# Kernel tuning notes

Measured on AMD Instinct MI355X. Metric: run time of the kernel, lower is better.

## Reference

```python
import jax, jax.numpy as jnp
import numpy as np

D_MODEL = 3072
N_HEADS = 24
MAX_LEN = 2048
ROPE_THETA = 10000.0
DH = D_MODEL // N_HEADS                  # 128
Q_PROJ = D_MODEL // 2                    # 1536
KV_PROJ = 2 * D_MODEL // 3               # 2048
NOPE = DH // 2                           # 64
ROPE = DH // 2                           # 64
EPS = 1e-5


def layernorm(x, w, b):
    m = jnp.mean(x, axis=-1, keepdims=True)
    v = jnp.mean(jnp.square(x - m), axis=-1, keepdims=True)
    return (x - m) / jnp.sqrt(v + EPS) * w + b


def rotate_half(x):
    h = x.shape[-1] // 2
    return jnp.concatenate([-x[..., h:], x[..., :h]], axis=-1)


def rope_tables(S):
    freqs = 1.0 / ROPE_THETA ** (jnp.arange(0, DH, 2, dtype=jnp.float32) / DH)  # [DH/2]
    emb = jnp.arange(S, dtype=jnp.float32)[:, None] * freqs[None, :]            # [S, DH/2]
    # torch: take first ROPE//2 freqs then .repeat(...,2) => tile along last axis
    cos = jnp.tile(jnp.cos(emb)[:, : ROPE // 2], (1, 2))  # [S, ROPE]
    sin = jnp.tile(jnp.sin(emb)[:, : ROPE // 2], (1, 2))
    return cos[None, None], sin[None, None]               # [1,1,S,ROPE]


def setup_inputs() -> dict:
    key = jax.random.key(0)
    ks = jax.random.split(key, 7)
    x = jax.random.normal(ks[0], (2, 2048, D_MODEL), dtype=jnp.float32)
    p = lambda k, shp: 0.01 * jax.random.normal(k, shp, dtype=jnp.float32)
    return {
        "x": x,
        "W_dq": p(ks[1], (D_MODEL, Q_PROJ)),
        "W_uq": p(ks[2], (Q_PROJ, D_MODEL)),
        "q_ln_w": jnp.ones((Q_PROJ,), jnp.float32),
        "q_ln_b": jnp.zeros((Q_PROJ,), jnp.float32),
        "W_dkv": p(ks[3], (D_MODEL, KV_PROJ + ROPE)),
        "W_ukv": p(ks[4], (KV_PROJ, D_MODEL + N_HEADS * NOPE)),
        "kv_ln_w": jnp.ones((KV_PROJ,), jnp.float32),
        "kv_ln_b": jnp.zeros((KV_PROJ,), jnp.float32),
        "W_o": p(ks[5], (D_MODEL, D_MODEL)),
    }


def reference(x, W_dq, W_uq, q_ln_w, q_ln_b, W_dkv, W_ukv, kv_ln_w, kv_ln_b, W_o):
    B, S, D = x.shape
    cos, sin = rope_tables(S)  # past_length=0, S_full=S

    # Q path: low-rank down/up projection
    cq = layernorm(x @ W_dq, q_ln_w, q_ln_b)          # [B,S,Q_PROJ]
    Q = (cq @ W_uq).reshape(B, S, N_HEADS, DH).transpose(0, 2, 1, 3)  # [B,H,S,DH]
    Q_nope, Q_rope = Q[..., :NOPE], Q[..., NOPE:]
    Q_rope = Q_rope * cos + rotate_half(Q_rope) * sin

    # KV path
    compressed_kv = x @ W_dkv                          # [B,S,KV_PROJ+ROPE]
    KV_lora = layernorm(compressed_kv[..., :KV_PROJ], kv_ln_w, kv_ln_b)
    K_rope = compressed_kv[..., KV_PROJ:]              # [B,S,ROPE]
    KV = (KV_lora @ W_ukv).reshape(B, S, N_HEADS, DH + NOPE).transpose(0, 2, 1, 3)
    K_nope, V = KV[..., :NOPE], KV[..., NOPE:]         # [B,H,S,NOPE], [B,H,S,DH]

    K_rope = K_rope[:, None]                           # [B,1,S,ROPE] shared head
    K_rope = K_rope * cos + rotate_half(K_rope) * sin

    q = jnp.concatenate([Q_nope, Q_rope], axis=-1)     # [B,H,S,DH]
    # k = cat(K_nope, K_rope broadcast over heads)
    k = jnp.concatenate([K_nope, jnp.broadcast_to(K_rope, (B, N_HEADS, S, ROPE))], axis=-1)

    scale = 1.0 / jnp.sqrt(jnp.float32(DH))
    scores = jnp.einsum("bhqd,bhkd->bhqk", q, k) * scale
    causal = jnp.tril(jnp.ones((S, S), dtype=bool))
    scores = jnp.where(causal[None, None], scores, jnp.float32(-jnp.inf))
    attn = jax.nn.softmax(scores, axis=-1)
    out = jnp.einsum("bhqk,bhkd->bhqd", attn, V)
    out = out.transpose(0, 2, 1, 3).reshape(B, S, D)
    out = out @ W_o.T
    return out, compressed_kv
```

## Files before the change

kernel.cpp:

```cpp
#include <hip/hip_runtime.h>

typedef unsigned short u16;
typedef __attribute__((ext_vector_type(8))) short short8;
typedef __attribute__((ext_vector_type(4))) float f32x4;

#define NROWS   4096
#define S_LEN   2048
#define NHEADS  24
#define DMODEL  3072
#define QPROJ   1536
#define KVPROJ  2048
#define CKV_W   2112
#define UKV_N   4608

__device__ __forceinline__ float bf2f(u16 v) {
    unsigned u = ((unsigned)v) << 16; float f; __builtin_memcpy(&f, &u, 4); return f;
}
__device__ __forceinline__ u16 f2bf(float f) {
    unsigned u; __builtin_memcpy(&u, &f, 4);
    u = (u + 0x7FFFu + ((u >> 16) & 1u)) >> 16; return (u16)u;
}
__device__ __forceinline__ void async16(const u16* g, u16* l) {
    __builtin_amdgcn_global_load_lds((const __attribute__((address_space(1))) unsigned int*)g,
                                     (__attribute__((address_space(3))) unsigned int*)l,
                                     16, 0, 0);
}

__global__ void conv_bf16(const float* __restrict__ X, u16* __restrict__ Y, int n) {
    int i = (blockIdx.x * 256 + threadIdx.x) * 4;
    if (i >= n) return;
    float4 v = *(const float4*)(X + i);
    Y[i+0] = f2bf(v.x); Y[i+1] = f2bf(v.y); Y[i+2] = f2bf(v.z); Y[i+3] = f2bf(v.w);
}

__global__ void transpose_bf16(const float* __restrict__ W, u16* __restrict__ WT,
                               int K, int N, float scale) {
    __shared__ float t[32][33];
    int nb = blockIdx.x * 32, kb = blockIdx.y * 32;
    int c = threadIdx.x & 31, rq = threadIdx.x >> 5;
#pragma unroll
    for (int i = 0; i < 4; ++i) {
        int r = rq * 4 + i;
        t[r][c] = W[(size_t)(kb + r) * N + nb + c];
    }
    __syncthreads();
#pragma unroll
    for (int i = 0; i < 4; ++i) {
        int r = rq * 4 + i;
        WT[(size_t)(nb + r) * K + kb + c] = f2bf(t[c][r] * scale);
    }
}

__global__ __launch_bounds__(256) void ln_kernel(const float* __restrict__ X, int ldx,
                                                 const float* __restrict__ g,
                                                 const float* __restrict__ b,
                                                 u16* __restrict__ Y, int W) {
    int row = blockIdx.x;
    const float4* x4 = (const float4*)(X + (size_t)row * ldx);
    int W4 = W >> 2;
    float s = 0.f, s2 = 0.f;
    for (int i = threadIdx.x; i < W4; i += 256) {
        float4 v = x4[i];
        s += v.x + v.y + v.z + v.w;
        s2 += v.x * v.x + v.y * v.y + v.z * v.z + v.w * v.w;
    }
#pragma unroll
    for (int off = 32; off >= 1; off >>= 1) { s += __shfl_xor(s, off); s2 += __shfl_xor(s2, off); }
    __shared__ float red[8];
    int w = threadIdx.x >> 6;
    if ((threadIdx.x & 63) == 0) { red[w] = s; red[4 + w] = s2; }
    __syncthreads();
    s  = red[0] + red[1] + red[2] + red[3];
    s2 = red[4] + red[5] + red[6] + red[7];
    float mean = s / W;
    float var  = s2 / W - mean * mean;
    float rstd = rsqrtf(var + 1e-5f);
    const float4* g4 = (const float4*)g;
    const float4* b4 = (const float4*)b;
    u16* y = Y + (size_t)row * W;
    for (int i = threadIdx.x; i < W4; i += 256) {
        float4 v = x4[i], gg = g4[i], bb = b4[i];
        u16 o[4];
        o[0] = f2bf((v.x - mean) * rstd * gg.x + bb.x);
        o[1] = f2bf((v.y - mean) * rstd * gg.y + bb.y);
        o[2] = f2bf((v.z - mean) * rstd * gg.z + bb.z);
        o[3] = f2bf((v.w - mean) * rstd * gg.w + bb.w);
        *(ulong1*)&y[i * 4] = *(ulong1*)o;
    }
}

__global__ void rope_q_kernel(u16* __restrict__ Q) {
    int idx = blockIdx.x * 256 + threadIdx.x;
    int j = idx & 31; int t = idx >> 5; int h = t % NHEADS; int row = t / NHEADS;
    int s = row & (S_LEN - 1);
    float freq = __expf(-(float)j * (9.210340371976184f / 64.f));
    float ang = (float)s * freq;
    float c = cosf(ang), si = sinf(ang);
    u16* p = Q + (size_t)row * DMODEL + h * 128 + 64;
    float x1 = bf2f(p[j]), x2 = bf2f(p[j + 32]);
    p[j]      = f2bf(x1 * c - x2 * si);
    p[j + 32] = f2bf(x2 * c + x1 * si);
}

__global__ void rope_k_kernel(const float* __restrict__ ckv, u16* __restrict__ kr) {
    int idx = blockIdx.x * 256 + threadIdx.x;
    int j = idx & 31; int row = idx >> 5;
    int s = row & (S_LEN - 1);
    float freq = __expf(-(float)j * (9.210340371976184f / 64.f));
    float ang = (float)s * freq;
    float c = cosf(ang), si = sinf(ang);
    const float* src = ckv + (size_t)row * CKV_W + KVPROJ;
    float x1 = src[j], x2 = src[j + 32];
    kr[(size_t)row * 64 + j]      = f2bf(x1 * c - x2 * si);
    kr[(size_t)row * 64 + j + 32] = f2bf(x2 * c + x1 * si);
}

__global__ __launch_bounds__(256) void pack_k(const u16* __restrict__ KVb,
                                              const u16* __restrict__ kr,
                                              u16* __restrict__ Kp) {
    int bh = blockIdx.y, bb = bh / NHEADS, h = bh % NHEADS;
    int s0 = blockIdx.x * 64;
    int t = threadIdx.x;
    size_t base = (size_t)bb * S_LEN;
#pragma unroll
    for (int it = 0; it < 4; ++it) {
        int j = it * 256 + t;
        int r = j >> 4, cb = (j & 15) * 8;
        int s = s0 + r;
        uint4 v;
        if (cb < 64) v = *(const uint4*)&KVb[(base + s) * UKV_N + h * 192 + cb];
        else         v = *(const uint4*)&kr[(base + s) * 64 + (cb - 64)];
        *(uint4*)&Kp[((size_t)bh * S_LEN + s) * 128 + cb] = v;
    }
}

__global__ __launch_bounds__(256) void pack_v(const u16* __restrict__ KVb,
                                              u16* __restrict__ Vt) {
    __shared__ u16 tile[64][136];
    int bh = blockIdx.y, bb = bh / NHEADS, h = bh % NHEADS;
    int s0 = blockIdx.x * 64;
    int t = threadIdx.x;
    size_t base = (size_t)bb * S_LEN;
#pragma unroll
    for (int it = 0; it < 4; ++it) {
        int j = it * 256 + t;
        int r = j >> 4, cb = (j & 15) * 8;
        *(uint4*)&tile[r][cb] = *(const uint4*)&KVb[(base + s0 + r) * UKV_N + h * 192 + 64 + cb];
    }
    __syncthreads();
#pragma unroll
    for (int it = 0; it < 4; ++it) {
        int j = it * 256 + t;
        int d = j >> 3, sb = (j & 7) * 8;
        u16 tmp[8];
#pragma unroll
        for (int e = 0; e < 8; ++e) tmp[e] = tile[sb + e][d];
        *(uint4*)&Vt[((size_t)bh * 128 + d) * S_LEN + s0 + sb] = *(uint4*)tmp;
    }
}

template<bool OUT_BF16>
__global__ __launch_bounds__(256) void gemm_nt(const u16* __restrict__ A,
                                               const u16* __restrict__ B,
                                               void* __restrict__ Cv,
                                               int M, int N, int K, int nx) {
    __shared__ u16 a_lds[2][128][32];
    __shared__ u16 b_lds[2][128][32];
    int nwg = (int)gridDim.x;
    int bid = (int)blockIdx.x;
    int wg = (bid & 7) * (nwg >> 3) + (bid >> 3);
    int by = wg / nx, bx = wg - by * nx;
    int m0 = by * 128, n0 = bx * 128;
    int tid = threadIdx.x, lane = tid & 63, w = tid >> 6;
    int wm = w >> 1, wn = w & 1;
    int srow = lane >> 2;
    int kx = (lane >> 4) & 2;
    int scol = ((lane & 3) ^ kx) * 8;
    int r0 = w * 32 + srow, r1 = w * 32 + 16 + srow;
    const u16* A0 = A + (size_t)(m0 + r0) * K + scol;
    const u16* A1 = A + (size_t)(m0 + r1) * K + scol;
    int bn0 = n0 + r0; if (bn0 >= N) bn0 = N - 1;
    int bn1 = n0 + r1; if (bn1 >= N) bn1 = N - 1;
    const u16* B0 = B + (size_t)bn0 * K + scol;
    const u16* B1 = B + (size_t)bn1 * K + scol;
    char* aB = (char*)&a_lds[0][0][0];
    char* bB = (char*)&b_lds[0][0][0];
    int d0 = w * 2048, d1 = w * 2048 + 1024;
    int cb = ((lane >> 4) * 16) ^ ((lane & 8) << 2);

    f32x4 acc[4][4] = {};
    async16(A0, (u16*)(aB + d0)); async16(A1, (u16*)(aB + d1));
    async16(B0, (u16*)(bB + d0)); async16(B1, (u16*)(bB + d1));
    __syncthreads();
    int buf = 0;
    for (int kb = 0; kb < K; kb += 32) {
        if (kb + 32 < K) {
            int ob = (buf ^ 1) * 8192;
            async16(A0 + kb + 32, (u16*)(aB + ob + d0));
            async16(A1 + kb + 32, (u16*)(aB + ob + d1));
            async16(B0 + kb + 32, (u16*)(bB + ob + d0));
            async16(B1 + kb + 32, (u16*)(bB + ob + d1));
        }
        const char* ab = aB + buf * 8192;
        const char* bb = bB + buf * 8192;
        short8 af[4], bf[4];
#pragma unroll
        for (int i = 0; i < 4; ++i) {
            af[i] = *(const short8*)(ab + (wm * 64 + i * 16 + (lane & 15)) * 64 + cb);
            bf[i] = *(const short8*)(bb + (wn * 64 + i * 16 + (lane & 15)) * 64 + cb);
        }
#pragma unroll
        for (int i = 0; i < 4; ++i)
#pragma unroll
            for (int j = 0; j < 4; ++j)
                acc[i][j] = __builtin_amdgcn_mfma_f32_16x16x32_bf16(af[i], bf[j], acc[i][j], 0, 0, 0);
        __syncthreads();
        buf ^= 1;
    }
#pragma unroll
    for (int i = 0; i < 4; ++i) {
        int row = m0 + wm * 64 + i * 16 + ((lane >> 4) << 2);
#pragma unroll
        for (int j = 0; j < 4; ++j) {
            int col = n0 + wn * 64 + j * 16 + (lane & 15);
            if (col < N) {
#pragma unroll
                for (int r = 0; r < 4; ++r) {
                    if (OUT_BF16) ((u16*)Cv)[(size_t)(row + r) * N + col] = f2bf(acc[i][j][r]);
                    else          ((float*)Cv)[(size_t)(row + r) * N + col] = acc[i][j][r];
                }
            }
        }
    }
}

__global__ __launch_bounds__(256) void attn_kernel(const u16* __restrict__ Qb,
                                                   const u16* __restrict__ Kp,
                                                   const u16* __restrict__ Vt,
                                                   u16* __restrict__ AO) {
    __shared__ u16 k_lds[64][128];
    __shared__ u16 v_lds[128][64];
    __shared__ u16 p_lds[4][16][64];
    int bid = blockIdx.x;
    int jj = bid >> 3;
    int bh = (bid & 7) * 6 + (jj >> 4);
    int bx = jj & 15;
    int bb = bh / NHEADS, h = bh % NHEADS;
    int tid = threadIdx.x, lane = tid & 63, w = tid >> 6;
    size_t base = (size_t)bb * S_LEN;
    size_t bhS = (size_t)bh * S_LEN;

    const char* Kbyte = (const char*)Kp;
    const char* Vbyte = (const char*)Vt;
    char* kB = (char*)&k_lds[0][0];
    char* vB = (char*)&v_lds[0][0];
    char* pB = (char*)&p_lds[0][0][0] + w * 2048;
    size_t ksrc[4], vsrc[4];
    int kd[4];
#pragma unroll
    for (int is = 0; is < 4; ++is) {
        int j = is * 256 + tid;
        int r = j >> 4;
        int cbs = ((j & 15) * 16) ^ ((r & 7) << 4);
        ksrc[is] = (bhS + r) * 256 + cbs;
        int d = j >> 3;
        int kbs = (((j & 7) ^ (d & 7)) * 16);
        vsrc[is] = ((size_t)bh * 128 + d) * (S_LEN * 2) + kbs;
        kd[is] = (is * 256 + w * 64) * 16;
    }

    for (int seg = 0; seg < 2; ++seg) {
        int qx = seg == 0 ? (31 - bx) : bx;
        int q0 = qx * 64;

        short8 qf[4];
        {
            int qrow = q0 + w * 16 + (lane & 15);
            const u16* qp = Qb + (base + qrow) * DMODEL + h * 128 + ((lane >> 4) * 8);
#pragma unroll
            for (int ks = 0; ks < 4; ++ks) qf[ks] = *(const short8*)(qp + ks * 32);
        }

        f32x4 acc_o[8] = {};
        float m_run[4], l_run[4];
#pragma unroll
        for (int r = 0; r < 4; ++r) { m_run[r] = -1e30f; l_run[r] = 0.f; }

        int ntiles = qx + 1;
        for (int t = 0; t < ntiles; ++t) {
            size_t kv0 = (size_t)t * 64;
#pragma unroll
            for (int is = 0; is < 4; ++is)
                async16((const u16*)(Kbyte + ksrc[is] + kv0 * 256), (u16*)(kB + kd[is]));
#pragma unroll
            for (int is = 0; is < 4; ++is)
                async16((const u16*)(Vbyte + vsrc[is] + kv0 * 2), (u16*)(vB + kd[is]));
            __syncthreads();

            f32x4 sc[4];
            __builtin_amdgcn_s_setprio(1);
#pragma unroll
            for (int nb = 0; nb < 4; ++nb) {
                f32x4 a = {};
                int row = nb * 16 + (lane & 15);
                const char* kb_ = kB + row * 256;
                int x = (row & 7) << 4;
#pragma unroll
                for (int ks = 0; ks < 4; ++ks) {
                    short8 kf = *(const short8*)(kb_ + ((ks * 64 + (lane >> 4) * 16) ^ x));
                    a = __builtin_amdgcn_mfma_f32_16x16x32_bf16(qf[ks], kf, a, 0, 0, 0);
                }
                sc[nb] = a;
            }
            __builtin_amdgcn_s_setprio(0);

            if (t == qx) {
                int kvb = t * 64;
                int qg = q0 + w * 16 + ((lane >> 4) << 2);
#pragma unroll
                for (int nb = 0; nb < 4; ++nb) {
                    int kc = kvb + nb * 16 + (lane & 15);
#pragma unroll
                    for (int r = 0; r < 4; ++r)
                        if (kc > qg + r) sc[nb][r] = -1e30f;
                }
            }
            float rmax[4];
#pragma unroll
            for (int r = 0; r < 4; ++r)
                rmax[r] = fmaxf(fmaxf(sc[0][r], sc[1][r]), fmaxf(sc[2][r], sc[3][r]));
#pragma unroll
            for (int off = 1; off < 16; off <<= 1)
#pragma unroll
                for (int r = 0; r < 4; ++r) rmax[r] = fmaxf(rmax[r], __shfl_xor(rmax[r], off));

            bool ok = (rmax[0] <= m_run[0]) & (rmax[1] <= m_run[1]) &
                      (rmax[2] <= m_run[2]) & (rmax[3] <= m_run[3]);
            if (!__all(ok)) {
                float fac[4];
#pragma unroll
                for (int r = 0; r < 4; ++r) {
                    float mnew = fmaxf(m_run[r], rmax[r]);
                    fac[r] = __expf(m_run[r] - mnew);
                    m_run[r] = mnew;
                    l_run[r] *= fac[r];
                }
#pragma unroll
                for (int db = 0; db < 8; ++db)
#pragma unroll
                    for (int r = 0; r < 4; ++r) acc_o[db][r] *= fac[r];
            }
#pragma unroll
            for (int nb = 0; nb < 4; ++nb)
#pragma unroll
                for (int r = 0; r < 4; ++r) {
                    float p = __expf(sc[nb][r] - m_run[r]);
                    sc[nb][r] = p; l_run[r] += p;
                }

#pragma unroll
            for (int nb = 0; nb < 4; ++nb)
#pragma unroll
                for (int r = 0; r < 4; ++r) {
                    int row = ((lane >> 4) << 2) + r;
                    int cby = (nb * 32 + (lane & 15) * 2) ^ ((row & 7) << 4);
                    *(u16*)(pB + row * 128 + cby) = f2bf(sc[nb][r]);
                }
            __builtin_amdgcn_sched_barrier(0);
            __builtin_amdgcn_s_setprio(1);
#pragma unroll
            for (int ks = 0; ks < 2; ++ks) {
                int prow = lane & 15;
                short8 pf = *(const short8*)(pB + prow * 128 +
                                ((ks * 64 + (lane >> 4) * 16) ^ ((prow & 7) << 4)));
#pragma unroll
                for (int db = 0; db < 8; ++db) {
                    int row = db * 16 + (lane & 15);
                    const char* vb_ = vB + row * 128;
                    short8 vf = *(const short8*)(vb_ + ((ks * 64 + (lane >> 4) * 16) ^ ((row & 7) << 4)));
                    acc_o[db] = __builtin_amdgcn_mfma_f32_16x16x32_bf16(pf, vf, acc_o[db], 0, 0, 0);
                }
            }
            __builtin_amdgcn_s_setprio(0);
            __syncthreads();
        }

#pragma unroll
        for (int off = 1; off < 16; off <<= 1)
#pragma unroll
            for (int r = 0; r < 4; ++r) l_run[r] += __shfl_xor(l_run[r], off);

        int orow = q0 + w * 16 + ((lane >> 4) << 2);
#pragma unroll
        for (int db = 0; db < 8; ++db)
#pragma unroll
            for (int r = 0; r < 4; ++r) {
                float o = acc_o[db][r] / l_run[r];
                AO[(base + orow + r) * DMODEL + h * 128 + db * 16 + (lane & 15)] = f2bf(o);
            }
    }
}

extern "C" void kernel_launch(void* const* d_in, const int* in_sizes, int n_in,
                              void* d_out, int out_size, void* d_ws, size_t ws_size,
                              hipStream_t stream) {
    (void)in_sizes; (void)n_in; (void)out_size; (void)ws_size;
    const float* x      = (const float*)d_in[0];
    const float* W_dq   = (const float*)d_in[1];
    const float* W_uq   = (const float*)d_in[2];
    const float* q_ln_w = (const float*)d_in[3];
    const float* q_ln_b = (const float*)d_in[4];
    const float* W_dkv  = (const float*)d_in[5];
    const float* W_ukv  = (const float*)d_in[6];
    const float* kv_ln_w= (const float*)d_in[7];
    const float* kv_ln_b= (const float*)d_in[8];
    const float* W_o    = (const float*)d_in[9];

    float* out = (float*)d_out;
    float* ckv = out + (size_t)NROWS * DMODEL;

    char* ws = (char*)d_ws;
    const size_t OFF_WDQT  = 0;
    const size_t OFF_WUQT  = 9437184;
    const size_t OFF_WDKVT = 18874368;
    const size_t OFF_WUKVT = 31850496;
    const size_t OFF_WO    = 50724864;
    const size_t OFF_XB    = 69599232;
    const size_t OFF_QB    = 94765056;
    const size_t OFF_KVB   = 119930880;
    const size_t OFF_KR    = 157679616;
    const size_t OFF_SLABA = 158203904;
    const size_t OFF_SLABB = 183369728;
    const size_t OFF_KP    = 0;
    const size_t OFF_VT    = OFF_XB;

    u16* Wdq_t  = (u16*)(ws + OFF_WDQT);
    u16* Wuq_t  = (u16*)(ws + OFF_WUQT);
    u16* Wdkv_t = (u16*)(ws + OFF_WDKVT);
    u16* Wukv_t = (u16*)(ws + OFF_WUKVT);
    u16* Wo_b   = (u16*)(ws + OFF_WO);
    u16* xb     = (u16*)(ws + OFF_XB);
    u16* qb     = (u16*)(ws + OFF_QB);
    u16* KVb    = (u16*)(ws + OFF_KVB);
    u16* kr     = (u16*)(ws + OFF_KR);
    float* t0   = (float*)(ws + OFF_SLABA);
    u16* ao     = (u16*)(ws + OFF_SLABA);
    u16* cq     = (u16*)(ws + OFF_SLABB);
    u16* kvl    = (u16*)(ws + OFF_SLABB);
    u16* Kp     = (u16*)(ws + OFF_KP);
    u16* Vt     = (u16*)(ws + OFF_VT);

    const float SCALE = 0.08838834764831845f;

    transpose_bf16<<<dim3(QPROJ / 32, DMODEL / 32), 256, 0, stream>>>(W_dq,  Wdq_t,  DMODEL, QPROJ, 1.0f);
    transpose_bf16<<<dim3(DMODEL / 32, QPROJ / 32), 256, 0, stream>>>(W_uq,  Wuq_t,  QPROJ, DMODEL, SCALE);
    transpose_bf16<<<dim3(CKV_W / 32, DMODEL / 32), 256, 0, stream>>>(W_dkv, Wdkv_t, DMODEL, CKV_W, 1.0f);
    transpose_bf16<<<dim3(UKV_N / 32, KVPROJ / 32), 256, 0, stream>>>(W_ukv, Wukv_t, KVPROJ, UKV_N, 1.0f);
    conv_bf16<<<9216, 256, 0, stream>>>(W_o, Wo_b, DMODEL * DMODEL);
    conv_bf16<<<12288, 256, 0, stream>>>(x, xb, NROWS * DMODEL);

    gemm_nt<false><<<(QPROJ / 128) * (NROWS / 128), 256, 0, stream>>>(xb, Wdq_t, t0, NROWS, QPROJ, DMODEL, QPROJ / 128);
    ln_kernel<<<NROWS, 256, 0, stream>>>(t0, QPROJ, q_ln_w, q_ln_b, cq, QPROJ);
    gemm_nt<true><<<(DMODEL / 128) * (NROWS / 128), 256, 0, stream>>>(cq, Wuq_t, qb, NROWS, DMODEL, QPROJ, DMODEL / 128);
    rope_q_kernel<<<12288, 256, 0, stream>>>(qb);

    gemm_nt<false><<<17 * (NROWS / 128), 256, 0, stream>>>(xb, Wdkv_t, ckv, NROWS, CKV_W, DMODEL, 17);
    ln_kernel<<<NROWS, 256, 0, stream>>>(ckv, CKV_W, kv_ln_w, kv_ln_b, kvl, KVPROJ);
    rope_k_kernel<<<512, 256, 0, stream>>>(ckv, kr);
    gemm_nt<true><<<(UKV_N / 128) * (NROWS / 128), 256, 0, stream>>>(kvl, Wukv_t, KVb, NROWS, UKV_N, KVPROJ, UKV_N / 128);

    pack_k<<<dim3(S_LEN / 64, 2 * NHEADS), 256, 0, stream>>>(KVb, kr, Kp);
    pack_v<<<dim3(S_LEN / 64, 2 * NHEADS), 256, 0, stream>>>(KVb, Vt);

    attn_kernel<<<768, 256, 0, stream>>>(qb, Kp, Vt, ao);

    gemm_nt<false><<<(DMODEL / 128) * (NROWS / 128), 256, 0, stream>>>(ao, Wo_b, out, NROWS, DMODEL, DMODEL, DMODEL / 128);
}
```

Baseline: 641.5 us.

## Add 256x256-tile 8-wave GEMM with 4-stage async pipeline for large projections

Adds a new NT GEMM kernel that uses 512 threads, 256x256 output tiles and a 4-slot LDS ring fed by async global-to-LDS loads, with loads interleaved between two MFMA half-phases and wave priority raised during MFMA. The up-projection GEMMs for Q and KV and the output projection now use it instead of the 128x128 kernel. The larger tiles are meant to raise arithmetic intensity and cut global/LDS traffic per FLOP, and the deeper pipeline is meant to hide load latency. In exchange the grid is much smaller (e.g. 192 or 288 workgroups), which risks tail and occupancy effects. The 128 KB LDS use also limits how many workgroups fit per CU.

```diff
diff --git a/kernel.cpp b/kernel.cpp
--- a/kernel.cpp
+++ b/kernel.cpp
@@ -234,6 +234,120 @@
     }
 }
 
+template<bool OUT_BF16>
+__global__ __launch_bounds__(512, 2) void gemm_nt8(const u16* __restrict__ A,
+                                                   const u16* __restrict__ B,
+                                                   void* __restrict__ Cv,
+                                                   int M, int N, int K, int nx) {
+    __shared__ u16 lds[4][2][256][32];
+    int nwg = (int)gridDim.x;
+    int bid = (int)blockIdx.x;
+    int wg = (bid & 7) * (nwg >> 3) + (bid >> 3);
+    int by = wg / nx, bx = wg - by * nx;
+    int m0 = by * 256, n0 = bx * 256;
+    int tid = threadIdx.x, lane = tid & 63, w = tid >> 6;
+    int wm = w >> 2, wn = w & 3;
+    char* L = (char*)&lds[0][0][0][0];
+
+    int ra = tid >> 2,          ca = ((tid & 3) ^ (ra & 3)) * 8;
+    int rb = (tid + 512) >> 2,  cbs = (((tid + 512) & 3) ^ (rb & 3)) * 8;
+    const u16* Asrc0 = A + (size_t)(m0 + ra) * K + ca;
+    const u16* Asrc1 = A + (size_t)(m0 + rb) * K + cbs;
+    const u16* Bsrc0 = B + (size_t)(n0 + ra) * K + ca;
+    const u16* Bsrc1 = B + (size_t)(n0 + rb) * K + cbs;
+    int dst0 = (w * 64) * 16;
+    int dst1 = 8192 + (w * 64) * 16;
+
+    int nkt = K >> 5;
+    f32x4 acc[8][4] = {};
+
+#pragma unroll
+    for (int k = 0; k < 3; ++k) {
+        int sb_ = (k & 3) * 32768;
+        async16(Asrc0 + k * 32, (u16*)(L + sb_ + dst0));
+        async16(Asrc1 + k * 32, (u16*)(L + sb_ + dst1));
+        async16(Bsrc0 + k * 32, (u16*)(L + sb_ + 16384 + dst0));
+        async16(Bsrc1 + k * 32, (u16*)(L + sb_ + 16384 + dst1));
+    }
+    asm volatile("s_waitcnt vmcnt(8)" ::: "memory");
+    __builtin_amdgcn_s_barrier();
+
+    for (int g = 0; g < nkt; ++g) {
+        int slot = g & 3;
+        const char* As = L + slot * 32768;
+        const char* Bs = L + slot * 32768 + 16384;
+        bool more = (g + 3 < nkt);
+        int s2 = ((g + 3) & 3) * 32768;
+        size_t koff = (size_t)(g + 3) * 32;
+
+        short8 bf[4];
+        if (more) {
+            async16(Asrc0 + koff, (u16*)(L + s2 + dst0));
+            async16(Asrc1 + koff, (u16*)(L + s2 + dst1));
+        }
+        {
+            short8 af[4];
+#pragma unroll
+            for (int f = 0; f < 4; ++f) {
+                int R = wm * 128 + f * 16 + (lane & 15);
+                af[f] = *(const short8*)(As + R * 64 + (((lane >> 4) * 16) ^ ((R & 3) << 4)));
+            }
+#pragma unroll
+            for (int nf = 0; nf < 4; ++nf) {
+                int R = wn * 64 + nf * 16 + (lane & 15);
+                bf[nf] = *(const short8*)(Bs + R * 64 + (((lane >> 4) * 16) ^ ((R & 3) << 4)));
+            }
+            __builtin_amdgcn_sched_barrier(0);
+            __builtin_amdgcn_s_barrier();
+            __builtin_amdgcn_s_setprio(1);
+#pragma unroll
+            for (int f = 0; f < 4; ++f)
+#pragma unroll
+                for (int nf = 0; nf < 4; ++nf)
+                    acc[f][nf] = __builtin_amdgcn_mfma_f32_16x16x32_bf16(af[f], bf[nf], acc[f][nf], 0, 0, 0);
+            __builtin_amdgcn_s_setprio(0);
+        }
+        if (more) {
+            async16(Bsrc0 + koff, (u16*)(L + s2 + 16384 + dst0));
+            async16(Bsrc1 + koff, (u16*)(L + s2 + 16384 + dst1));
+        }
+        {
+            short8 af[4];
+#pragma unroll
+            for (int f = 0; f < 4; ++f) {
+                int R = wm * 128 + 64 + f * 16 + (lane & 15);
+                af[f] = *(const short8*)(As + R * 64 + (((lane >> 4) * 16) ^ ((R & 3) << 4)));
+            }
+            __builtin_amdgcn_sched_barrier(0);
+            __builtin_amdgcn_s_barrier();
+            __builtin_amdgcn_s_setprio(1);
+#pragma unroll
+            for (int f = 0; f < 4; ++f)
+#pragma unroll
+                for (int nf = 0; nf < 4; ++nf)
+                    acc[4 + f][nf] = __builtin_amdgcn_mfma_f32_16x16x32_bf16(af[f], bf[nf], acc[4 + f][nf], 0, 0, 0);
+            __builtin_amdgcn_s_setprio(0);
+        }
+        if (more) asm volatile("s_waitcnt vmcnt(8)" ::: "memory");
+        else      asm volatile("s_waitcnt vmcnt(0)" ::: "memory");
+        __builtin_amdgcn_s_barrier();
+    }
+
+#pragma unroll
+    for (int mi = 0; mi < 8; ++mi) {
+        int row = m0 + wm * 128 + mi * 16 + ((lane >> 4) << 2);
+#pragma unroll
+        for (int nf = 0; nf < 4; ++nf) {
+            int col = n0 + wn * 64 + nf * 16 + (lane & 15);
+#pragma unroll
+            for (int r = 0; r < 4; ++r) {
+                if (OUT_BF16) ((u16*)Cv)[(size_t)(row + r) * N + col] = f2bf(acc[mi][nf][r]);
+                else          ((float*)Cv)[(size_t)(row + r) * N + col] = acc[mi][nf][r];
+            }
+        }
+    }
+}
+
 __global__ __launch_bounds__(256) void attn_kernel(const u16* __restrict__ Qb,
                                                    const u16* __restrict__ Kp,
                                                    const u16* __restrict__ Vt,
@@ -461,18 +575,18 @@
 
     gemm_nt<false><<<(QPROJ / 128) * (NROWS / 128), 256, 0, stream>>>(xb, Wdq_t, t0, NROWS, QPROJ, DMODEL, QPROJ / 128);
     ln_kernel<<<NROWS, 256, 0, stream>>>(t0, QPROJ, q_ln_w, q_ln_b, cq, QPROJ);
-    gemm_nt<true><<<(DMODEL / 128) * (NROWS / 128), 256, 0, stream>>>(cq, Wuq_t, qb, NROWS, DMODEL, QPROJ, DMODEL / 128);
+    gemm_nt8<true><<<(DMODEL / 256) * (NROWS / 256), 512, 0, stream>>>(cq, Wuq_t, qb, NROWS, DMODEL, QPROJ, DMODEL / 256);
     rope_q_kernel<<<12288, 256, 0, stream>>>(qb);
 
     gemm_nt<false><<<17 * (NROWS / 128), 256, 0, stream>>>(xb, Wdkv_t, ckv, NROWS, CKV_W, DMODEL, 17);
     ln_kernel<<<NROWS, 256, 0, stream>>>(ckv, CKV_W, kv_ln_w, kv_ln_b, kvl, KVPROJ);
     rope_k_kernel<<<512, 256, 0, stream>>>(ckv, kr);
-    gemm_nt<true><<<(UKV_N / 128) * (NROWS / 128), 256, 0, stream>>>(kvl, Wukv_t, KVb, NROWS, UKV_N, KVPROJ, UKV_N / 128);
+    gemm_nt8<true><<<(UKV_N / 256) * (NROWS / 256), 512, 0, stream>>>(kvl, Wukv_t, KVb, NROWS, UKV_N, KVPROJ, UKV_N / 256);
 
     pack_k<<<dim3(S_LEN / 64, 2 * NHEADS), 256, 0, stream>>>(KVb, kr, Kp);
     pack_v<<<dim3(S_LEN / 64, 2 * NHEADS), 256, 0, stream>>>(KVb, Vt);
 
     attn_kernel<<<768, 256, 0, stream>>>(qb, Kp, Vt, ao);
 
-    gemm_nt<false><<<(DMODEL / 128) * (NROWS / 128), 256, 0, stream>>>(ao, Wo_b, out, NROWS, DMODEL, DMODEL, DMODEL / 128);
-}
+    gemm_nt8<false><<<(DMODEL / 256) * (NROWS / 256), 512, 0, stream>>>(ao, Wo_b, out, NROWS, DMODEL, DMODEL, DMODEL / 256);
+}
```

Result: no change. 651.6 us (+1.6%).
